# Optimization experiments

Hardware: AMD Instinct MI355X
Metric: run time of the kernel (lower is better)

## Reference

```python
import jax, jax.numpy as jnp
import numpy as np

THR = 0.2
BORDER_RM = 2
TEMP = 0.1


def _border_valid(n, b):
    idx = jnp.arange(n)
    return (idx >= b) & (idx < n - b)


def setup_inputs() -> dict:
    key = jax.random.key(0)
    k0, k1 = jax.random.split(key)
    N, L, S, C = 4, 3600, 3600, 256
    return {
        "feat_c0": jax.random.normal(k0, (N, L, C), dtype=jnp.float32),
        "feat_c1": jax.random.normal(k1, (N, S, C), dtype=jnp.float32),
        "h0c": 60, "w0c": 60, "h1c": 60, "w1c": 60,
    }


def reference(feat_c0, feat_c1, h0c, w0c, h1c, w1c):
    N, L, C = feat_c0.shape
    S = feat_c1.shape[1]
    inv_sqrt_c = 1.0 / (C ** 0.5)
    f0 = feat_c0 * inv_sqrt_c
    f1 = feat_c1 * inv_sqrt_c
    # [N, L, S] similarity, temperature 0.1
    sim = jnp.einsum('nlc,nsc->nls', f0, f1) / TEMP
    conf = jax.nn.softmax(sim, axis=1) * jax.nn.softmax(sim, axis=2)

    # threshold mask + border removal (applied in [b,h0,w0,h1,w1] layout,
    # expressed here as separable 1D validity masks -- same result, no 5D copy churn)
    v0h = _border_valid(h0c, BORDER_RM)  # [h0c]
    v0w = _border_valid(w0c, BORDER_RM)
    v1h = _border_valid(h1c, BORDER_RM)
    v1w = _border_valid(w1c, BORDER_RM)
    valid_l = (v0h[:, None] & v0w[None, :]).reshape(L)   # [L]
    valid_s = (v1h[:, None] & v1w[None, :]).reshape(S)   # [S]
    mask = (conf > THR) & valid_l[None, :, None] & valid_s[None, None, :]

    # mutual nearest (dual argmax equality)
    mask = mask & (conf == conf.max(axis=2, keepdims=True)) & (conf == conf.max(axis=1, keepdims=True))

    # fixed-shape match extraction: per (b, i) row, is there a match and where
    mask_v = jnp.any(mask, axis=2)                       # [N, L] bool
    all_j_ids = jnp.argmax(mask, axis=2)                 # [N, L] int
    mconf = jnp.take_along_axis(conf, all_j_ids[:, :, None], axis=2)[:, :, 0]
    mconf = jnp.where(mask_v, mconf, 0.0)                # [N, L]
    return conf, mask_v, all_j_ids, mconf
```

## Files before the change

kernel.cpp:

```cpp
#include <hip/hip_runtime.h>
#include <stdint.h>


typedef _Float16 f16;
typedef _Float16 f16x8 __attribute__((ext_vector_type(8)));
typedef float f32x4 __attribute__((ext_vector_type(4)));

#define N_B 4
#define L_DIM 3600
#define S_DIM 3600
#define C_DIM 256
#define BM 48
#define BN 48
#define WAVES 3
#define NTHREADS 192
#define CHUNK_COLS 720
#define CHUNK_ITERS 15
#define NCHUNKS 5
#define NRT 75
#define YT_STRIDE 264

#define C_EXP1 (0.0390625f * 1.4426950408889634f)
#define C_EXP2 (2.0f * 0.0390625f * 1.4426950408889634f)

__global__ void cast_kernel(const float* __restrict__ a, const float* __restrict__ b,
                            f16* __restrict__ ah, f16* __restrict__ bh, int total8) {
  int i = blockIdx.x * blockDim.x + threadIdx.x;
  if (i >= total8) return;
  const float4* a4 = (const float4*)a;
  const float4* b4 = (const float4*)b;
  float4 x = a4[2 * (size_t)i], y = a4[2 * (size_t)i + 1];
  f16x8 o = {(f16)x.x, (f16)x.y, (f16)x.z, (f16)x.w,
             (f16)y.x, (f16)y.y, (f16)y.z, (f16)y.w};
  *(f16x8*)(ah + 8 * (size_t)i) = o;
  x = b4[2 * (size_t)i]; y = b4[2 * (size_t)i + 1];
  f16x8 o2 = {(f16)x.x, (f16)x.y, (f16)x.z, (f16)x.w,
              (f16)y.x, (f16)y.y, (f16)y.z, (f16)y.w};
  *(f16x8*)(bh + 8 * (size_t)i) = o2;
}

__global__ __launch_bounds__(NTHREADS) void stats_kernel(
    const f16* __restrict__ X, const f16* __restrict__ Y, float* __restrict__ den) {
  __shared__ f16 Yt[BN][YT_STRIDE];
  const int rt = blockIdx.x, ch = blockIdx.y, n = blockIdx.z;
  const int tid = threadIdx.x;
  const int wave = tid >> 6, lane = tid & 63;
  const int q = lane >> 4, r = lane & 15;
  const int l0 = rt * BM;
  const int s0 = ch * CHUNK_COLS;

  f16x8 a[8];
  {
    const f16* xrow = X + ((size_t)n * L_DIM + l0 + wave * 16 + r) * C_DIM;
#pragma unroll
    for (int k = 0; k < 8; ++k) a[k] = *(const f16x8*)(xrow + k * 32 + q * 8);
  }

  float sum_e[4] = {0.f, 0.f, 0.f, 0.f};

  for (int it = 0; it < CHUNK_ITERS; ++it) {
    const f16* ysrc = Y + ((size_t)n * S_DIM + s0 + it * BN) * C_DIM;
#pragma unroll
    for (int i = 0; i < 8; ++i) {
      int c = i * NTHREADS + tid;
      int row = c >> 5, cc = c & 31;
      *(f16x8*)&Yt[row][cc * 8] = *(const f16x8*)(ysrc + row * C_DIM + cc * 8);
    }
    __syncthreads();

    f32x4 acc[3];
#pragma unroll
    for (int t = 0; t < 3; ++t) acc[t] = (f32x4){0.f, 0.f, 0.f, 0.f};
#pragma unroll
    for (int nt = 0; nt < 3; ++nt) {
#pragma unroll
      for (int k = 0; k < 8; ++k) {
        f16x8 b = *(const f16x8*)&Yt[nt * 16 + r][k * 32 + q * 8];
        acc[nt] = __builtin_amdgcn_mfma_f32_16x16x32_f16(a[k], b, acc[nt], 0, 0, 0);
      }
    }
    __syncthreads();

#pragma unroll
    for (int nt = 0; nt < 3; ++nt)
#pragma unroll
      for (int g = 0; g < 4; ++g) sum_e[g] += exp2f(acc[nt][g] * C_EXP1);
  }

#pragma unroll
  for (int m = 1; m < 16; m <<= 1)
#pragma unroll
    for (int g = 0; g < 4; ++g) sum_e[g] += __shfl_xor(sum_e[g], m, 64);
  if (r == 0) {
#pragma unroll
    for (int g = 0; g < 4; ++g)
      atomicAdd(&den[n * L_DIM + l0 + wave * 16 + q * 4 + g], sum_e[g]);
  }
}

__global__ void invert_kernel(float* __restrict__ a, float* __restrict__ b) {
  int i = blockIdx.x * blockDim.x + threadIdx.x;
  if (i >= N_B * L_DIM) return;
  a[i] = 1.0f / a[i];
  b[i] = 1.0f / b[i];
}

__global__ __launch_bounds__(NTHREADS) void conf_kernel(
    const f16* __restrict__ X, const f16* __restrict__ Y,
    const float* __restrict__ invdr, const float* __restrict__ invdc,
    float* __restrict__ conf_out, unsigned long long* __restrict__ rowarg,
    float* __restrict__ colpart) {
  __shared__ f16 Yt[BN][YT_STRIDE];
  __shared__ float cmax_w[WAVES][CHUNK_COLS];
  const int rt = blockIdx.x, ch = blockIdx.y, n = blockIdx.z;
  const int tid = threadIdx.x;
  const int wave = tid >> 6, lane = tid & 63;
  const int q = lane >> 4, r = lane & 15;
  const int l0 = rt * BM;
  const int s0 = ch * CHUNK_COLS;

  f16x8 a[8];
  {
    const f16* xrow = X + ((size_t)n * L_DIM + l0 + wave * 16 + r) * C_DIM;
#pragma unroll
    for (int k = 0; k < 8; ++k) a[k] = *(const f16x8*)(xrow + k * 32 + q * 8);
  }
  float idr[4];
#pragma unroll
  for (int g = 0; g < 4; ++g)
    idr[g] = invdr[n * L_DIM + l0 + wave * 16 + q * 4 + g];

  float rmax[4] = {0.f, 0.f, 0.f, 0.f};
  int rj[4] = {0, 0, 0, 0};

  for (int it = 0; it < CHUNK_ITERS; ++it) {
    const f16* ysrc = Y + ((size_t)n * S_DIM + s0 + it * BN) * C_DIM;
#pragma unroll
    for (int i = 0; i < 8; ++i) {
      int c = i * NTHREADS + tid;
      int row = c >> 5, cc = c & 31;
      *(f16x8*)&Yt[row][cc * 8] = *(const f16x8*)(ysrc + row * C_DIM + cc * 8);
    }
    __syncthreads();

    f32x4 acc[3];
#pragma unroll
    for (int t = 0; t < 3; ++t) acc[t] = (f32x4){0.f, 0.f, 0.f, 0.f};
#pragma unroll
    for (int nt = 0; nt < 3; ++nt) {
#pragma unroll
      for (int k = 0; k < 8; ++k) {
        f16x8 b = *(const f16x8*)&Yt[nt * 16 + r][k * 32 + q * 8];
        acc[nt] = __builtin_amdgcn_mfma_f32_16x16x32_f16(a[k], b, acc[nt], 0, 0, 0);
      }
    }
    __syncthreads();

#pragma unroll
    for (int nt = 0; nt < 3; ++nt) {
      int scol = s0 + it * BN + nt * 16 + r;
      float idc = invdc[n * S_DIM + scol];
      float cm = 0.f;
#pragma unroll
      for (int g = 0; g < 4; ++g) {
        float v = exp2f(acc[nt][g] * C_EXP2) * idr[g] * idc;
        int lrow = l0 + wave * 16 + q * 4 + g;
        conf_out[((size_t)n * L_DIM + lrow) * S_DIM + scol] = v;
        if (v > rmax[g]) { rmax[g] = v; rj[g] = scol; }
        cm = fmaxf(cm, v);
      }
      cm = fmaxf(cm, __shfl_xor(cm, 16, 64));
      cm = fmaxf(cm, __shfl_xor(cm, 32, 64));
      if (q == 0) cmax_w[wave][it * BN + nt * 16 + r] = cm;
    }
  }

#pragma unroll
  for (int m = 1; m < 16; m <<= 1) {
#pragma unroll
    for (int g = 0; g < 4; ++g) {
      float ov = __shfl_xor(rmax[g], m, 64);
      int oj = __shfl_xor(rj[g], m, 64);
      if (ov > rmax[g] || (ov == rmax[g] && oj < rj[g])) { rmax[g] = ov; rj[g] = oj; }
    }
  }
  if (r == 0) {
#pragma unroll
    for (int g = 0; g < 4; ++g) {
      unsigned long long key =
          ((unsigned long long)__float_as_uint(rmax[g]) << 32) |
          (unsigned int)(~(unsigned int)rj[g]);
      atomicMax(&rowarg[n * L_DIM + l0 + wave * 16 + q * 4 + g], key);
    }
  }

  __syncthreads();
  for (int i = tid; i < CHUNK_COLS; i += NTHREADS) {
    float p = fmaxf(fmaxf(cmax_w[0][i], cmax_w[1][i]), cmax_w[2][i]);
    colpart[((size_t)n * NRT + rt) * S_DIM + s0 + i] = p;
  }
}

__global__ void colmerge_kernel(const float* __restrict__ colpart,
                                float* __restrict__ colmax) {
  int i = blockIdx.x * blockDim.x + threadIdx.x;
  if (i >= N_B * S_DIM) return;
  int n = i / S_DIM, s = i - n * S_DIM;
  float m = 0.f;
  for (int rt = 0; rt < NRT; ++rt)
    m = fmaxf(m, colpart[((size_t)n * NRT + rt) * S_DIM + s]);
  colmax[i] = m;
}

__global__ void finalize_kernel(const unsigned long long* __restrict__ rowarg,
                                const float* __restrict__ colmax,
                                const int* __restrict__ h0c, const int* __restrict__ w0c,
                                const int* __restrict__ h1c, const int* __restrict__ w1c,
                                float* __restrict__ out_maskv, float* __restrict__ out_jids,
                                float* __restrict__ out_mconf) {
  int i = blockIdx.x * blockDim.x + threadIdx.x;
  if (i >= N_B * L_DIM) return;
  int n = i / L_DIM, l = i - n * L_DIM;
  unsigned long long key = rowarg[i];
  float rm = __uint_as_float((unsigned int)(key >> 32));
  int j = (int)(~(unsigned int)key);
  int W0 = *w0c, H0 = *h0c, W1 = *w1c, H1 = *h1c;
  int li = l / W0, lj = l - li * W0;
  bool vl = (li >= 2) && (li < H0 - 2) && (lj >= 2) && (lj < W0 - 2);
  int si = j / W1, sj = j - si * W1;
  bool vs = (si >= 2) && (si < H1 - 2) && (sj >= 2) && (sj < W1 - 2);
  float cm = colmax[n * S_DIM + j];
  bool mv = (rm > 0.2f) && vl && vs &&
            (__float_as_uint(rm) == __float_as_uint(cm));
  out_maskv[i] = mv ? 1.0f : 0.0f;
  out_jids[i]  = mv ? (float)j : 0.0f;
  out_mconf[i] = mv ? rm : 0.0f;
}

extern "C" void kernel_launch(void* const* d_in, const int* in_sizes, int n_in,
                              void* d_out, int out_size, void* d_ws, size_t ws_size,
                              hipStream_t stream) {
  const float* f0 = (const float*)d_in[0];
  const float* f1 = (const float*)d_in[1];
  const int* h0c = (const int*)d_in[2];
  const int* w0c = (const int*)d_in[3];
  const int* h1c = (const int*)d_in[4];
  const int* w1c = (const int*)d_in[5];

  char* ws = (char*)d_ws;
  size_t o = 0;
  f16* f0h = (f16*)(ws + o);               o += (size_t)N_B * L_DIM * C_DIM * 2;
  f16* f1h = (f16*)(ws + o);               o += (size_t)N_B * S_DIM * C_DIM * 2;
  float* den_r = (float*)(ws + o);         o += (size_t)N_B * L_DIM * 4;
  float* den_c = (float*)(ws + o);         o += (size_t)N_B * S_DIM * 4;
  unsigned long long* rowarg = (unsigned long long*)(ws + o); o += (size_t)N_B * L_DIM * 8;
  float* colmax = (float*)(ws + o);        o += (size_t)N_B * S_DIM * 4;
  float* colpart = (float*)(ws + o);       o += (size_t)N_B * NRT * S_DIM * 4;

  float* conf = (float*)d_out;
  float* out_maskv = conf + (size_t)N_B * L_DIM * S_DIM;
  float* out_jids = out_maskv + N_B * L_DIM;
  float* out_mconf = out_jids + N_B * L_DIM;

  hipMemsetAsync(den_r, 0, (size_t)N_B * L_DIM * 4, stream);
  hipMemsetAsync(den_c, 0, (size_t)N_B * S_DIM * 4, stream);
  hipMemsetAsync(rowarg, 0, (size_t)N_B * L_DIM * 8, stream);

  int total8 = N_B * L_DIM * C_DIM / 8;
  cast_kernel<<<dim3((total8 + 255) / 256), 256, 0, stream>>>(f0, f1, f0h, f1h, total8);

  dim3 grid(NRT, NCHUNKS, N_B);
  stats_kernel<<<grid, NTHREADS, 0, stream>>>(f0h, f1h, den_r);
  stats_kernel<<<grid, NTHREADS, 0, stream>>>(f1h, f0h, den_c);
  invert_kernel<<<(N_B * L_DIM + 255) / 256, 256, 0, stream>>>(den_r, den_c);
  conf_kernel<<<grid, NTHREADS, 0, stream>>>(f0h, f1h, den_r, den_c, conf, rowarg, colpart);
  colmerge_kernel<<<(N_B * S_DIM + 255) / 256, 256, 0, stream>>>(colpart, colmax);
  finalize_kernel<<<(N_B * L_DIM + 255) / 256, 256, 0, stream>>>(
      rowarg, colmax, h0c, w0c, h1c, w1c, out_maskv, out_jids, out_mconf);
}
```

Measured before the change: 435.1 us.

## Fuse stats GEMMs into one pass storing exp tile, square it for conf

Replaces the two separate row/column stats GEMMs and the recomputing conf GEMM with one GEMM pass. That pass stores exp(sim/2T) as f16 and accumulates both row and column denominators through atomics. A streaming conf kernel then squares the stored values and normalizes them, removing two of the three GEMMs at the cost of writing and reading a large f16 intermediate. Storing in f16 reduces precision for conf and argmax ties. The GEMM row tile is also enlarged to 144 rows per block to reuse Y tiles.

After: 414.4 us. -4.7%, faster.

```diff
diff --git a/kernel.cpp b/kernel.cpp
--- a/kernel.cpp
+++ b/kernel.cpp
@@ -4,24 +4,27 @@
 
 typedef _Float16 f16;
 typedef _Float16 f16x8 __attribute__((ext_vector_type(8)));
+typedef _Float16 f16x4 __attribute__((ext_vector_type(4)));
 typedef float f32x4 __attribute__((ext_vector_type(4)));
 
 #define N_B 4
 #define L_DIM 3600
 #define S_DIM 3600
 #define C_DIM 256
-#define BM 48
-#define BN 48
-#define WAVES 3
-#define NTHREADS 192
-#define CHUNK_COLS 720
-#define CHUNK_ITERS 15
-#define NCHUNKS 5
-#define NRT 75
+
+#define P1_THREADS 192
+#define P1_BM 144
+#define P1_BN 48
+#define P1_ITERS 15
+#define P1_CHUNK 720
+#define P1_NCH 5
+#define P1_NRT 25
 #define YT_STRIDE 264
 
+#define P2_ROWS 48
+#define P2_NRT 75
+
 #define C_EXP1 (0.0390625f * 1.4426950408889634f)
-#define C_EXP2 (2.0f * 0.0390625f * 1.4426950408889634f)
 
 __global__ void cast_kernel(const float* __restrict__ a, const float* __restrict__ b,
                             f16* __restrict__ ah, f16* __restrict__ bh, int total8) {
@@ -39,63 +42,100 @@
   *(f16x8*)(bh + 8 * (size_t)i) = o2;
 }
 
-__global__ __launch_bounds__(NTHREADS) void stats_kernel(
-    const f16* __restrict__ X, const f16* __restrict__ Y, float* __restrict__ den) {
-  __shared__ f16 Yt[BN][YT_STRIDE];
+__global__ __launch_bounds__(P1_THREADS) void gemm_stats_kernel(
+    const f16* __restrict__ X, const f16* __restrict__ Y,
+    f16* __restrict__ eh, float* __restrict__ den_r, float* __restrict__ den_c) {
+  __shared__ f16 Yt[P1_BN][YT_STRIDE];
+  __shared__ float colsum_w[3][P1_CHUNK];
   const int rt = blockIdx.x, ch = blockIdx.y, n = blockIdx.z;
   const int tid = threadIdx.x;
   const int wave = tid >> 6, lane = tid & 63;
   const int q = lane >> 4, r = lane & 15;
-  const int l0 = rt * BM;
-  const int s0 = ch * CHUNK_COLS;
-
-  f16x8 a[8];
-  {
-    const f16* xrow = X + ((size_t)n * L_DIM + l0 + wave * 16 + r) * C_DIM;
-#pragma unroll
-    for (int k = 0; k < 8; ++k) a[k] = *(const f16x8*)(xrow + k * 32 + q * 8);
-  }
-
-  float sum_e[4] = {0.f, 0.f, 0.f, 0.f};
-
-  for (int it = 0; it < CHUNK_ITERS; ++it) {
-    const f16* ysrc = Y + ((size_t)n * S_DIM + s0 + it * BN) * C_DIM;
+  const int l0 = rt * P1_BM;
+  const int s0 = ch * P1_CHUNK;
+
+  f16x8 a[3][8];
+#pragma unroll
+  for (int grp = 0; grp < 3; ++grp) {
+    const f16* xrow = X + ((size_t)n * L_DIM + l0 + wave * 48 + grp * 16 + r) * C_DIM;
+#pragma unroll
+    for (int k = 0; k < 8; ++k) a[grp][k] = *(const f16x8*)(xrow + k * 32 + q * 8);
+  }
+
+  float sum_e[3][4];
+#pragma unroll
+  for (int grp = 0; grp < 3; ++grp)
+#pragma unroll
+    for (int g = 0; g < 4; ++g) sum_e[grp][g] = 0.f;
+
+  const f16* ebase = eh + ((size_t)n * L_DIM + l0 + wave * 48) * S_DIM;
+
+  for (int it = 0; it < P1_ITERS; ++it) {
+    const f16* ysrc = Y + ((size_t)n * S_DIM + s0 + it * P1_BN) * C_DIM;
 #pragma unroll
     for (int i = 0; i < 8; ++i) {
-      int c = i * NTHREADS + tid;
+      int c = i * P1_THREADS + tid;
       int row = c >> 5, cc = c & 31;
       *(f16x8*)&Yt[row][cc * 8] = *(const f16x8*)(ysrc + row * C_DIM + cc * 8);
     }
     __syncthreads();
 
-    f32x4 acc[3];
-#pragma unroll
-    for (int t = 0; t < 3; ++t) acc[t] = (f32x4){0.f, 0.f, 0.f, 0.f};
+    f32x4 acc[3][3];
+#pragma unroll
+    for (int grp = 0; grp < 3; ++grp)
+#pragma unroll
+      for (int nt = 0; nt < 3; ++nt) acc[grp][nt] = (f32x4){0.f, 0.f, 0.f, 0.f};
+
+#pragma unroll
+    for (int k = 0; k < 8; ++k) {
+#pragma unroll
+      for (int nt = 0; nt < 3; ++nt) {
+        f16x8 b = *(const f16x8*)&Yt[nt * 16 + r][k * 32 + q * 8];
+#pragma unroll
+        for (int grp = 0; grp < 3; ++grp)
+          acc[grp][nt] = __builtin_amdgcn_mfma_f32_16x16x32_f16(a[grp][k], b, acc[grp][nt], 0, 0, 0);
+      }
+    }
+    __syncthreads();
+
 #pragma unroll
     for (int nt = 0; nt < 3; ++nt) {
-#pragma unroll
-      for (int k = 0; k < 8; ++k) {
-        f16x8 b = *(const f16x8*)&Yt[nt * 16 + r][k * 32 + q * 8];
-        acc[nt] = __builtin_amdgcn_mfma_f32_16x16x32_f16(a[k], b, acc[nt], 0, 0, 0);
+      int scol = s0 + it * P1_BN + nt * 16 + r;
+      float csum = 0.f;
+#pragma unroll
+      for (int grp = 0; grp < 3; ++grp) {
+#pragma unroll
+        for (int g = 0; g < 4; ++g) {
+          float e = exp2f(acc[grp][nt][g] * C_EXP1);
+          sum_e[grp][g] += e;
+          csum += e;
+          ((f16*)ebase)[(size_t)(grp * 16 + q * 4 + g) * S_DIM + scol] = (f16)e;
+        }
       }
-    }
-    __syncthreads();
-
-#pragma unroll
-    for (int nt = 0; nt < 3; ++nt)
-#pragma unroll
-      for (int g = 0; g < 4; ++g) sum_e[g] += exp2f(acc[nt][g] * C_EXP1);
+      csum += __shfl_xor(csum, 16, 64);
+      csum += __shfl_xor(csum, 32, 64);
+      if (q == 0) colsum_w[wave][it * P1_BN + nt * 16 + r] = csum;
+    }
   }
 
 #pragma unroll
   for (int m = 1; m < 16; m <<= 1)
 #pragma unroll
-    for (int g = 0; g < 4; ++g) sum_e[g] += __shfl_xor(sum_e[g], m, 64);
+    for (int grp = 0; grp < 3; ++grp)
+#pragma unroll
+      for (int g = 0; g < 4; ++g) sum_e[grp][g] += __shfl_xor(sum_e[grp][g], m, 64);
   if (r == 0) {
 #pragma unroll
-    for (int g = 0; g < 4; ++g)
-      atomicAdd(&den[n * L_DIM + l0 + wave * 16 + q * 4 + g], sum_e[g]);
-  }
+    for (int grp = 0; grp < 3; ++grp)
+#pragma unroll
+      for (int g = 0; g < 4; ++g)
+        atomicAdd(&den_r[n * L_DIM + l0 + wave * 48 + grp * 16 + q * 4 + g], sum_e[grp][g]);
+  }
+
+  __syncthreads();
+  for (int i = tid; i < P1_CHUNK; i += P1_THREADS)
+    atomicAdd(&den_c[n * S_DIM + s0 + i],
+              colsum_w[0][i] + colsum_w[1][i] + colsum_w[2][i]);
 }
 
 __global__ void invert_kernel(float* __restrict__ a, float* __restrict__ b) {
@@ -105,100 +145,75 @@
   b[i] = 1.0f / b[i];
 }
 
-__global__ __launch_bounds__(NTHREADS) void conf_kernel(
-    const f16* __restrict__ X, const f16* __restrict__ Y,
-    const float* __restrict__ invdr, const float* __restrict__ invdc,
-    float* __restrict__ conf_out, unsigned long long* __restrict__ rowarg,
-    float* __restrict__ colpart) {
-  __shared__ f16 Yt[BN][YT_STRIDE];
-  __shared__ float cmax_w[WAVES][CHUNK_COLS];
-  const int rt = blockIdx.x, ch = blockIdx.y, n = blockIdx.z;
+__global__ __launch_bounds__(256) void conf_kernel(
+    const f16* __restrict__ eh, const float* __restrict__ invdr,
+    const float* __restrict__ invdc, float* __restrict__ conf_out,
+    unsigned long long* __restrict__ rowarg, float* __restrict__ colpart) {
+  const int rt = blockIdx.x, n = blockIdx.y;
   const int tid = threadIdx.x;
   const int wave = tid >> 6, lane = tid & 63;
-  const int q = lane >> 4, r = lane & 15;
-  const int l0 = rt * BM;
-  const int s0 = ch * CHUNK_COLS;
-
-  f16x8 a[8];
-  {
-    const f16* xrow = X + ((size_t)n * L_DIM + l0 + wave * 16 + r) * C_DIM;
-#pragma unroll
-    for (int k = 0; k < 8; ++k) a[k] = *(const f16x8*)(xrow + k * 32 + q * 8);
-  }
-  float idr[4];
-#pragma unroll
-  for (int g = 0; g < 4; ++g)
-    idr[g] = invdr[n * L_DIM + l0 + wave * 16 + q * 4 + g];
-
-  float rmax[4] = {0.f, 0.f, 0.f, 0.f};
-  int rj[4] = {0, 0, 0, 0};
-
-  for (int it = 0; it < CHUNK_ITERS; ++it) {
-    const f16* ysrc = Y + ((size_t)n * S_DIM + s0 + it * BN) * C_DIM;
-#pragma unroll
-    for (int i = 0; i < 8; ++i) {
-      int c = i * NTHREADS + tid;
-      int row = c >> 5, cc = c & 31;
-      *(f16x8*)&Yt[row][cc * 8] = *(const f16x8*)(ysrc + row * C_DIM + cc * 8);
-    }
-    __syncthreads();
-
-    f32x4 acc[3];
-#pragma unroll
-    for (int t = 0; t < 3; ++t) acc[t] = (f32x4){0.f, 0.f, 0.f, 0.f};
-#pragma unroll
-    for (int nt = 0; nt < 3; ++nt) {
-#pragma unroll
-      for (int k = 0; k < 8; ++k) {
-        f16x8 b = *(const f16x8*)&Yt[nt * 16 + r][k * 32 + q * 8];
-        acc[nt] = __builtin_amdgcn_mfma_f32_16x16x32_f16(a[k], b, acc[nt], 0, 0, 0);
+  const int l0 = rt * P2_ROWS;
+
+  int colb[4];
+  bool cv[4];
+  float4 idc4[4];
+  float4 cp[4];
+#pragma unroll
+  for (int ci = 0; ci < 4; ++ci) {
+    int chunk = ci * 64 + lane;
+    cv[ci] = chunk < 225;
+    colb[ci] = (wave * 225 + (chunk < 225 ? chunk : 0)) * 4;
+    idc4[ci] = *(const float4*)(invdc + n * S_DIM + colb[ci]);
+    cp[ci] = (float4){0.f, 0.f, 0.f, 0.f};
+  }
+
+  for (int row = 0; row < P2_ROWS; ++row) {
+    const int l = l0 + row;
+    const f16* erow = eh + ((size_t)n * L_DIM + l) * S_DIM;
+    float* crow = conf_out + ((size_t)n * L_DIM + l) * S_DIM;
+    const float idr = invdr[n * L_DIM + l];
+    float mx = 0.f;
+    int mj = 0;
+#pragma unroll
+    for (int ci = 0; ci < 4; ++ci) {
+      if (cv[ci]) {
+        f16x4 e4 = *(const f16x4*)(erow + colb[ci]);
+        float e0 = (float)e4.x, e1 = (float)e4.y, e2 = (float)e4.z, e3 = (float)e4.w;
+        float4 w;
+        w.x = e0 * e0 * idr * idc4[ci].x;
+        w.y = e1 * e1 * idr * idc4[ci].y;
+        w.z = e2 * e2 * idr * idc4[ci].z;
+        w.w = e3 * e3 * idr * idc4[ci].w;
+        *(float4*)(crow + colb[ci]) = w;
+        int c0 = colb[ci];
+        if (w.x > mx) { mx = w.x; mj = c0; }
+        if (w.y > mx) { mx = w.y; mj = c0 + 1; }
+        if (w.z > mx) { mx = w.z; mj = c0 + 2; }
+        if (w.w > mx) { mx = w.w; mj = c0 + 3; }
+        cp[ci].x = fmaxf(cp[ci].x, w.x);
+        cp[ci].y = fmaxf(cp[ci].y, w.y);
+        cp[ci].z = fmaxf(cp[ci].z, w.z);
+        cp[ci].w = fmaxf(cp[ci].w, w.w);
       }
     }
-    __syncthreads();
-
-#pragma unroll
-    for (int nt = 0; nt < 3; ++nt) {
-      int scol = s0 + it * BN + nt * 16 + r;
-      float idc = invdc[n * S_DIM + scol];
-      float cm = 0.f;
-#pragma unroll
-      for (int g = 0; g < 4; ++g) {
-        float v = exp2f(acc[nt][g] * C_EXP2) * idr[g] * idc;
-        int lrow = l0 + wave * 16 + q * 4 + g;
-        conf_out[((size_t)n * L_DIM + lrow) * S_DIM + scol] = v;
-        if (v > rmax[g]) { rmax[g] = v; rj[g] = scol; }
-        cm = fmaxf(cm, v);
-      }
-      cm = fmaxf(cm, __shfl_xor(cm, 16, 64));
-      cm = fmaxf(cm, __shfl_xor(cm, 32, 64));
-      if (q == 0) cmax_w[wave][it * BN + nt * 16 + r] = cm;
-    }
-  }
-
-#pragma unroll
-  for (int m = 1; m < 16; m <<= 1) {
-#pragma unroll
-    for (int g = 0; g < 4; ++g) {
-      float ov = __shfl_xor(rmax[g], m, 64);
-      int oj = __shfl_xor(rj[g], m, 64);
-      if (ov > rmax[g] || (ov == rmax[g] && oj < rj[g])) { rmax[g] = ov; rj[g] = oj; }
-    }
-  }
-  if (r == 0) {
-#pragma unroll
-    for (int g = 0; g < 4; ++g) {
+#pragma unroll
+    for (int m = 1; m < 64; m <<= 1) {
+      float ov = __shfl_xor(mx, m, 64);
+      int oj = __shfl_xor(mj, m, 64);
+      if (ov > mx || (ov == mx && oj < mj)) { mx = ov; mj = oj; }
+    }
+    if (lane == 0) {
       unsigned long long key =
-          ((unsigned long long)__float_as_uint(rmax[g]) << 32) |
-          (unsigned int)(~(unsigned int)rj[g]);
-      atomicMax(&rowarg[n * L_DIM + l0 + wave * 16 + q * 4 + g], key);
-    }
-  }
-
-  __syncthreads();
-  for (int i = tid; i < CHUNK_COLS; i += NTHREADS) {
-    float p = fmaxf(fmaxf(cmax_w[0][i], cmax_w[1][i]), cmax_w[2][i]);
-    colpart[((size_t)n * NRT + rt) * S_DIM + s0 + i] = p;
-  }
+          ((unsigned long long)__float_as_uint(mx) << 32) |
+          (unsigned int)(~(unsigned int)mj);
+      atomicMax(&rowarg[n * L_DIM + l], key);
+    }
+  }
+
+  float* cpo = colpart + ((size_t)n * P2_NRT + rt) * S_DIM;
+#pragma unroll
+  for (int ci = 0; ci < 4; ++ci)
+    if (cv[ci]) *(float4*)(cpo + colb[ci]) = cp[ci];
 }
 
 __global__ void colmerge_kernel(const float* __restrict__ colpart,
@@ -207,8 +222,8 @@
   if (i >= N_B * S_DIM) return;
   int n = i / S_DIM, s = i - n * S_DIM;
   float m = 0.f;
-  for (int rt = 0; rt < NRT; ++rt)
-    m = fmaxf(m, colpart[((size_t)n * NRT + rt) * S_DIM + s]);
+  for (int rt = 0; rt < P2_NRT; ++rt)
+    m = fmaxf(m, colpart[((size_t)n * P2_NRT + rt) * S_DIM + s]);
   colmax[i] = m;
 }
 
@@ -254,26 +269,26 @@
   float* den_r = (float*)(ws + o);         o += (size_t)N_B * L_DIM * 4;
   float* den_c = (float*)(ws + o);         o += (size_t)N_B * S_DIM * 4;
   unsigned long long* rowarg = (unsigned long long*)(ws + o); o += (size_t)N_B * L_DIM * 8;
+  size_t zero_bytes = (size_t)N_B * L_DIM * (4 + 4 + 8);
   float* colmax = (float*)(ws + o);        o += (size_t)N_B * S_DIM * 4;
-  float* colpart = (float*)(ws + o);       o += (size_t)N_B * NRT * S_DIM * 4;
+  float* colpart = (float*)(ws + o);       o += (size_t)N_B * P2_NRT * S_DIM * 4;
+  f16* eh = (f16*)(ws + o);                o += (size_t)N_B * L_DIM * S_DIM * 2;
 
   float* conf = (float*)d_out;
   float* out_maskv = conf + (size_t)N_B * L_DIM * S_DIM;
   float* out_jids = out_maskv + N_B * L_DIM;
   float* out_mconf = out_jids + N_B * L_DIM;
 
-  hipMemsetAsync(den_r, 0, (size_t)N_B * L_DIM * 4, stream);
-  hipMemsetAsync(den_c, 0, (size_t)N_B * S_DIM * 4, stream);
-  hipMemsetAsync(rowarg, 0, (size_t)N_B * L_DIM * 8, stream);
+  hipMemsetAsync(den_r, 0, zero_bytes, stream);
 
   int total8 = N_B * L_DIM * C_DIM / 8;
   cast_kernel<<<dim3((total8 + 255) / 256), 256, 0, stream>>>(f0, f1, f0h, f1h, total8);
 
-  dim3 grid(NRT, NCHUNKS, N_B);
-  stats_kernel<<<grid, NTHREADS, 0, stream>>>(f0h, f1h, den_r);
-  stats_kernel<<<grid, NTHREADS, 0, stream>>>(f1h, f0h, den_c);
+  dim3 g1(P1_NRT, P1_NCH, N_B);
+  gemm_stats_kernel<<<g1, P1_THREADS, 0, stream>>>(f0h, f1h, eh, den_r, den_c);
   invert_kernel<<<(N_B * L_DIM + 255) / 256, 256, 0, stream>>>(den_r, den_c);
-  conf_kernel<<<grid, NTHREADS, 0, stream>>>(f0h, f1h, den_r, den_c, conf, rowarg, colpart);
+  dim3 g2(P2_NRT, N_B);
+  conf_kernel<<<g2, 256, 0, stream>>>(eh, den_r, den_c, conf, rowarg, colpart);
   colmerge_kernel<<<(N_B * S_DIM + 255) / 256, 256, 0, stream>>>(colpart, colmax);
   finalize_kernel<<<(N_B * L_DIM + 255) / 256, 256, 0, stream>>>(
       rowarg, colmax, h0c, w0c, h1c, w1c, out_maskv, out_jids, out_mconf);
```
